# Optimization experiments

Measured on AMD Instinct MI355X. Metric: run time of the kernel, lower is better.

The kernel has to match this reference:

```python
import jax, jax.numpy as jnp
import numpy as np

DIM = 512
HEADS = 8
DK = DIM // HEADS
MAX_LEN = 22118
EPS = 1e-5


def _layernorm(h, g, b):
    m = jnp.mean(h, axis=-1, keepdims=True)
    v = jnp.mean((h - m) ** 2, axis=-1, keepdims=True)
    return (h - m) / jnp.sqrt(v + EPS) * g + b


def setup_inputs() -> dict:
    key = jax.random.key(0)
    ks = jax.random.split(key, 16)
    B, S = 4, 2048
    xavier = lambda k, shp: jax.random.normal(k, shp, jnp.float32) * np.sqrt(2.0 / (shp[0] + shp[1]))
    return {
        "x": jax.random.normal(ks[0], (B, S, DIM), jnp.float32),
        "vis_data": jax.random.normal(ks[1], (B, S, DIM), jnp.float32),
        "coord1": jax.random.randint(ks[2], (B, S), 0, MAX_LEN, jnp.int32),
        "coord2": jax.random.randint(ks[3], (B, S), 0, MAX_LEN, jnp.int32),
        "emb1": jax.random.normal(ks[4], (MAX_LEN, DIM // 2), jnp.float32) * 0.02,
        "emb2": jax.random.normal(ks[5], (MAX_LEN, DIM // 2), jnp.float32) * 0.02,
        "wq": xavier(ks[6], (DIM, DIM)), "bq": jnp.zeros((DIM,), jnp.float32),
        "wk": xavier(ks[7], (DIM, DIM)), "bk": jnp.zeros((DIM,), jnp.float32),
        "wv": xavier(ks[8], (DIM, DIM)), "bv": jnp.zeros((DIM,), jnp.float32),
        "w1": xavier(ks[9], (DIM, DIM)), "b1": jnp.zeros((DIM,), jnp.float32),
        "g1": jnp.ones((DIM,), jnp.float32), "beta1": jnp.zeros((DIM,), jnp.float32),
        "w2": xavier(ks[10], (DIM, DIM)), "b2": jnp.zeros((DIM,), jnp.float32),
        "g2": jnp.ones((DIM,), jnp.float32), "beta2": jnp.zeros((DIM,), jnp.float32),
    }


def reference(x, vis_data, coord1, coord2, emb1, emb2, wq, bq, wk, bk, wv, bv,
              w1, b1, g1, beta1, w2, b2, g2, beta2):
    B, S, _ = x.shape
    # learned positional encoding: concat of two coordinate embeddings
    pos = jnp.concatenate([emb1[coord1], emb2[coord2]], axis=-1)  # [B,S,DIM]
    xp = x + pos
    # Q/K from vis_data, V from position-encoded x
    q = (vis_data @ wq + bq).reshape(B, S, HEADS, DK)
    k = (vis_data @ wk + bk).reshape(B, S, HEADS, DK)
    v = (xp @ wv + bv).reshape(B, S, HEADS, DK)
    scores = jnp.einsum("bqhd,bkhd->bhqk", q, k) / np.sqrt(DK).astype(np.float32)
    attn = jax.nn.softmax(scores, axis=-1)  # dropout is identity in eval
    out = jnp.einsum("bhqk,bkhd->bqhd", attn, v).reshape(B, S, DIM)
    # post-attention MLP stack (self.layer)
    h = jax.nn.leaky_relu(out @ w1 + b1, negative_slope=0.2)
    h = _layernorm(h, g1, beta1)
    h = jax.nn.leaky_relu(h @ w2 + b2, negative_slope=0.2)
    h = _layernorm(h, g2, beta2)
    return h
```

## Files before the change

kernel.cpp:

```cpp
#include <hip/hip_runtime.h>

#define DIM 512
#define SEQ 2048
#define MROWS 8192

typedef short short8 __attribute__((ext_vector_type(8)));
typedef float floatx4 __attribute__((ext_vector_type(4)));

__device__ __forceinline__ ushort f2bf(float f) {
  union { float f; unsigned u; } v; v.f = f;
  unsigned r = v.u + 0x7fff + ((v.u >> 16) & 1);
  return (ushort)(r >> 16);
}
__device__ __forceinline__ float bf2f(ushort u) {
  union { unsigned u; float f; } v; v.u = ((unsigned)u) << 16;
  return v.f;
}

__global__ __launch_bounds__(256) void prep_kernel(
    const float* __restrict__ x, const float* __restrict__ vis,
    const int* __restrict__ c1, const int* __restrict__ c2,
    const float* __restrict__ e1, const float* __restrict__ e2,
    ushort* __restrict__ xp_bf, ushort* __restrict__ vis_bf) {
  int gid = blockIdx.x * 256 + threadIdx.x;
  int row = gid >> 7;
  int col = (gid & 127) * 4;
  float4 vv = *(const float4*)(vis + (size_t)row * 512 + col);
  ushort4 vb; vb.x = f2bf(vv.x); vb.y = f2bf(vv.y); vb.z = f2bf(vv.z); vb.w = f2bf(vv.w);
  *(ushort4*)(vis_bf + (size_t)row * 512 + col) = vb;
  float4 p;
  if (col < 256) p = *(const float4*)(e1 + (size_t)c1[row] * 256 + col);
  else           p = *(const float4*)(e2 + (size_t)c2[row] * 256 + col - 256);
  float4 xv = *(const float4*)(x + (size_t)row * 512 + col);
  ushort4 xb; xb.x = f2bf(xv.x + p.x); xb.y = f2bf(xv.y + p.y);
  xb.z = f2bf(xv.z + p.z); xb.w = f2bf(xv.w + p.w);
  *(ushort4*)(xp_bf + (size_t)row * 512 + col) = xb;
}

__global__ __launch_bounds__(256) void wtrans_kernel(
    const float* __restrict__ wq, const float* __restrict__ wk,
    const float* __restrict__ wv, const float* __restrict__ w1,
    const float* __restrict__ w2,
    ushort* __restrict__ wt_qkv, ushort* __restrict__ wt1,
    ushort* __restrict__ wt2) {
  __shared__ float Ls[64 * 65];
  int mid = blockIdx.x >> 6;
  int tile = blockIdx.x & 63;
  int k0 = (tile >> 3) * 64, n0 = (tile & 7) * 64;
  const float* W = mid == 0 ? wq : mid == 1 ? wk : mid == 2 ? wv : mid == 3 ? w1 : w2;
  ushort* outp = mid < 3 ? (wt_qkv + (size_t)mid * 512 * 512) : (mid == 3 ? wt1 : wt2);
  float scale = (mid == 0) ? 0.125f : 1.0f;
  int r = threadIdx.x >> 4, c4 = (threadIdx.x & 15) * 4;
#pragma unroll
  for (int i = 0; i < 4; i++) {
    int row = i * 16 + r;
    float4 wv4 = *(const float4*)(W + (size_t)(k0 + row) * 512 + n0 + c4);
    Ls[row * 65 + c4 + 0] = wv4.x * scale;
    Ls[row * 65 + c4 + 1] = wv4.y * scale;
    Ls[row * 65 + c4 + 2] = wv4.z * scale;
    Ls[row * 65 + c4 + 3] = wv4.w * scale;
  }
  __syncthreads();
  int n = threadIdx.x >> 2, kc = (threadIdx.x & 3) * 16;
  ushort pk[16];
#pragma unroll
  for (int i = 0; i < 16; i++) pk[i] = f2bf(Ls[(kc + i) * 65 + n]);
  ushort* op = outp + (size_t)(n0 + n) * 512 + k0 + kc;
  *(uint4*)op = *(uint4*)pk;
  *(uint4*)(op + 8) = *(uint4*)(pk + 8);
}

template <bool LEAKY>
__global__ __launch_bounds__(256, 3) void gemm_mfma(
    const ushort* __restrict__ A01, const ushort* __restrict__ A2,
    const ushort* __restrict__ Wt,
    const float* __restrict__ bias0, const float* __restrict__ bias1,
    const float* __restrict__ bias2,
    ushort* __restrict__ out0, ushort* __restrict__ out1,
    ushort* __restrict__ out2, float s0scale) {
  __shared__ __align__(16) ushort As[128 * 64];
  __shared__ __align__(16) ushort Bs[128 * 64];
  int t = threadIdx.x;
  int seg = blockIdx.x >> 2;
  int nloc0 = (blockIdx.x & 3) * 128;
  int n0w = blockIdx.x * 128;
  int m0 = blockIdx.y * 128;
  const ushort* A = (seg < 2) ? A01 : A2;
  const float* bias = seg == 0 ? bias0 : seg == 1 ? bias1 : bias2;
  ushort* out = seg == 0 ? out0 : seg == 1 ? out1 : out2;
  float bscale = seg == 0 ? s0scale : 1.0f;

  int w = t >> 6, lane = t & 63;
  int wm = (w & 1) * 64, wn = (w >> 1) * 64;
  int quad = lane >> 4, lcol = lane & 15;
  int srow = t >> 3, sch = t & 7;

  floatx4 acc[4][4] = {};

  for (int k0 = 0; k0 < 512; k0 += 64) {
    __syncthreads();
#pragma unroll
    for (int i = 0; i < 4; i++) {
      int row = i * 32 + srow;
      int pofs = row * 64 + (sch ^ (row & 7)) * 8;
      *(uint4*)(&As[pofs]) =
          *(const uint4*)(A + (size_t)(m0 + row) * 512 + k0 + sch * 8);
      *(uint4*)(&Bs[pofs]) =
          *(const uint4*)(Wt + (size_t)(n0w + row) * 512 + k0 + sch * 8);
    }
    __syncthreads();
#pragma unroll
    for (int kc = 0; kc < 2; kc++) {
      int pch = ((kc * 4 + quad) ^ (lcol & 7)) * 8;
      short8 af[4], bfr[4];
#pragma unroll
      for (int i = 0; i < 4; i++) {
        af[i]  = *(const short8*)(&As[(wm + i * 16 + lcol) * 64 + pch]);
        bfr[i] = *(const short8*)(&Bs[(wn + i * 16 + lcol) * 64 + pch]);
      }
#pragma unroll
      for (int mt = 0; mt < 4; mt++)
#pragma unroll
        for (int nt = 0; nt < 4; nt++)
          acc[mt][nt] = __builtin_amdgcn_mfma_f32_16x16x32_bf16(
              af[mt], bfr[nt], acc[mt][nt], 0, 0, 0);
    }
  }

  __syncthreads();
  float* Ls = ((w & 2) ? (float*)Bs : (float*)As) + (w & 1) * 1104;
  int rr = lane >> 2, cc = (lane & 3) * 16;
#pragma unroll
  for (int mt = 0; mt < 4; mt++) {
#pragma unroll
    for (int nt = 0; nt < 4; nt++) {
      float bv = bias[nloc0 + wn + nt * 16 + lcol] * bscale;
#pragma unroll
      for (int r = 0; r < 4; r++) {
        float vv = acc[mt][nt][r] + bv;
        if (LEAKY) vv = vv >= 0.f ? vv : 0.2f * vv;
        Ls[(quad * 4 + r) * 68 + nt * 16 + lcol] = vv;
      }
    }
    asm volatile("s_waitcnt lgkmcnt(0)" ::: "memory");
    ushort pk[16];
#pragma unroll
    for (int i = 0; i < 16; i += 4) {
      float4 fv = *(const float4*)(&Ls[rr * 68 + cc + i]);
      pk[i] = f2bf(fv.x); pk[i + 1] = f2bf(fv.y);
      pk[i + 2] = f2bf(fv.z); pk[i + 3] = f2bf(fv.w);
    }
    ushort* op = out + (size_t)(m0 + wm + mt * 16 + rr) * 512 + nloc0 + wn + cc;
    *(uint4*)op = *(uint4*)pk;
    *(uint4*)(op + 8) = *(uint4*)(pk + 8);
    asm volatile("s_waitcnt lgkmcnt(0)" ::: "memory");
  }
}

__global__ __launch_bounds__(256, 4) void attn_mfma_kernel(
    const ushort* __restrict__ q, const ushort* __restrict__ k,
    const ushort* __restrict__ v, ushort* __restrict__ out) {
  __shared__ __align__(16) ushort Ks[128 * 64];
  __shared__ __align__(16) ushort Vt[64 * 128];
  __shared__ __align__(16) ushort Ps[4 * 16 * 64];
  int t = threadIdx.x;
  int blk = blockIdx.x;
  int qt = blk & 31, h = (blk >> 5) & 7, b = blk >> 8;
  int wave = t >> 6, lane = t & 63, quad = lane >> 4, lcol = lane & 15;
  int q0 = qt * 64 + wave * 16;
  const size_t base = (size_t)b * SEQ * 512 + h * 64;

  short8 qf[2];
#pragma unroll
  for (int kc = 0; kc < 2; kc++)
    qf[kc] = *(const short8*)(q + base + (size_t)(q0 + lcol) * 512 + kc * 32 + quad * 8);

  floatx4 O[4] = {};
  float lsum[4] = {0.f, 0.f, 0.f, 0.f};

  ushort* Pw = Ps + wave * (16 * 64);
  int krow = t >> 1, khalf = t & 1;
  int pl = t & 63, dg = t >> 6;

  for (int kt = 0; kt < SEQ; kt += 128) {
    __syncthreads();
#pragma unroll
    for (int j = 0; j < 4; j++) {
      int ch = khalf * 4 + j;
      *(uint4*)(&Ks[krow * 64 + (ch ^ (krow & 7)) * 8]) =
          *(const uint4*)(k + base + (size_t)(kt + krow) * 512 + ch * 8);
    }
    {
      uint4 va[2], vb[2];
      const ushort* vr0 = v + base + (size_t)(kt + 2 * pl) * 512 + dg * 16;
      const ushort* vr1 = vr0 + 512;
      va[0] = *(const uint4*)(vr0); va[1] = *(const uint4*)(vr0 + 8);
      vb[0] = *(const uint4*)(vr1); vb[1] = *(const uint4*)(vr1 + 8);
      const ushort* a0 = (const ushort*)va;
      const ushort* a1 = (const ushort*)vb;
#pragma unroll
      for (int i = 0; i < 16; i++) {
        int dim = dg * 16 + i;
        unsigned pack = (unsigned)a0[i] | ((unsigned)a1[i] << 16);
        int pch = (pl >> 2) ^ (dim & 7);
        *(unsigned*)(&Vt[dim * 128 + pch * 8 + (pl & 3) * 2]) = pack;
      }
    }
    __syncthreads();

    floatx4 S[8] = {};
#pragma unroll
    for (int kc = 0; kc < 2; kc++) {
      int pch = ((kc * 4 + quad) ^ (lcol & 7)) * 8;
#pragma unroll
      for (int jt = 0; jt < 8; jt++) {
        short8 kf = *(const short8*)(&Ks[(jt * 16 + lcol) * 64 + pch]);
        S[jt] = __builtin_amdgcn_mfma_f32_16x16x32_bf16(qf[kc], kf, S[jt], 0, 0, 0);
      }
    }

#pragma unroll
    for (int half = 0; half < 2; half++) {
#pragma unroll
      for (int jt4 = 0; jt4 < 4; jt4++) {
        int jt = half * 4 + jt4;
#pragma unroll
        for (int r = 0; r < 4; r++) {
          float p = __expf(S[jt][r]);
          lsum[r] += p;
          int prow = quad * 4 + r;
          int pcol = jt4 * 16 + lcol;
          int pch = (pcol >> 3) ^ (prow & 7);
          Pw[prow * 64 + pch * 8 + (pcol & 7)] =
              (ushort)(__float_as_uint(p) >> 16);
        }
      }
      asm volatile("s_waitcnt lgkmcnt(0)" ::: "memory");
#pragma unroll
      for (int kc = 0; kc < 2; kc++) {
        short8 pf = *(const short8*)(
            &Pw[lcol * 64 + ((kc * 4 + quad) ^ (lcol & 7)) * 8]);
#pragma unroll
        for (int nt = 0; nt < 4; nt++) {
          int dim = nt * 16 + lcol;
          int ch = half * 8 + kc * 4 + quad;
          short8 vf = *(const short8*)(&Vt[dim * 128 + (ch ^ (lcol & 7)) * 8]);
          O[nt] = __builtin_amdgcn_mfma_f32_16x16x32_bf16(pf, vf, O[nt], 0, 0, 0);
        }
      }
    }
  }

#pragma unroll
  for (int r = 0; r < 4; r++) {
#pragma unroll
    for (int m = 1; m <= 8; m <<= 1) lsum[r] += __shfl_xor(lsum[r], m, 64);
    lsum[r] = 1.f / lsum[r];
  }
#pragma unroll
  for (int nt = 0; nt < 4; nt++)
#pragma unroll
    for (int r = 0; r < 4; r++)
      out[base + (size_t)(q0 + quad * 4 + r) * 512 + nt * 16 + lcol] =
          f2bf(O[nt][r] * lsum[r]);
}

template <bool OUTF32>
__global__ __launch_bounds__(256) void ln_kernel(
    const ushort* __restrict__ h, const float* __restrict__ g,
    const float* __restrict__ beta, void* __restrict__ outv) {
  int wave = threadIdx.x >> 6, lane = threadIdx.x & 63;
  int row = blockIdx.x * 4 + wave;
  uint4 raw = *(const uint4*)(h + (size_t)row * 512 + lane * 8);
  const ushort* hu = (const ushort*)&raw;
  float vals[8];
#pragma unroll
  for (int i = 0; i < 8; i++) vals[i] = bf2f(hu[i]);
  float sum = 0.f;
#pragma unroll
  for (int i = 0; i < 8; i++) sum += vals[i];
#pragma unroll
  for (int off = 32; off >= 1; off >>= 1) sum += __shfl_xor(sum, off, 64);
  float mean = sum * (1.f / 512.f);
  float vs = 0.f;
#pragma unroll
  for (int i = 0; i < 8; i++) { float d = vals[i] - mean; vs += d * d; }
#pragma unroll
  for (int off = 32; off >= 1; off >>= 1) vs += __shfl_xor(vs, off, 64);
  float rstd = rsqrtf(vs * (1.f / 512.f) + 1e-5f);
  float4 gv0 = *(const float4*)(g + lane * 8);
  float4 gv1 = *(const float4*)(g + lane * 8 + 4);
  float4 bv0 = *(const float4*)(beta + lane * 8);
  float4 bv1 = *(const float4*)(beta + lane * 8 + 4);
  float gr[8] = {gv0.x, gv0.y, gv0.z, gv0.w, gv1.x, gv1.y, gv1.z, gv1.w};
  float br[8] = {bv0.x, bv0.y, bv0.z, bv0.w, bv1.x, bv1.y, bv1.z, bv1.w};
  float res[8];
#pragma unroll
  for (int i = 0; i < 8; i++) res[i] = (vals[i] - mean) * rstd * gr[i] + br[i];
  if (OUTF32) {
    float* op = (float*)outv + (size_t)row * 512 + lane * 8;
    float4 o0, o1;
    o0.x = res[0]; o0.y = res[1]; o0.z = res[2]; o0.w = res[3];
    o1.x = res[4]; o1.y = res[5]; o1.z = res[6]; o1.w = res[7];
    *(float4*)op = o0; *(float4*)(op + 4) = o1;
  } else {
    ushort* op = (ushort*)outv + (size_t)row * 512 + lane * 8;
    ushort4 o0, o1;
    o0.x = f2bf(res[0]); o0.y = f2bf(res[1]); o0.z = f2bf(res[2]); o0.w = f2bf(res[3]);
    o1.x = f2bf(res[4]); o1.y = f2bf(res[5]); o1.z = f2bf(res[6]); o1.w = f2bf(res[7]);
    *(ushort4*)op = o0; *(ushort4*)(op + 4) = o1;
  }
}

extern "C" void kernel_launch(void* const* d_in, const int* in_sizes, int n_in,
                              void* d_out, int out_size, void* d_ws,
                              size_t ws_size, hipStream_t stream) {
  (void)in_sizes; (void)n_in; (void)out_size; (void)ws_size;
  const float* x     = (const float*)d_in[0];
  const float* vis   = (const float*)d_in[1];
  const int*   c1    = (const int*)d_in[2];
  const int*   c2    = (const int*)d_in[3];
  const float* e1    = (const float*)d_in[4];
  const float* e2    = (const float*)d_in[5];
  const float* wq    = (const float*)d_in[6];
  const float* bq    = (const float*)d_in[7];
  const float* wk    = (const float*)d_in[8];
  const float* bk    = (const float*)d_in[9];
  const float* wv    = (const float*)d_in[10];
  const float* bv    = (const float*)d_in[11];
  const float* w1    = (const float*)d_in[12];
  const float* b1    = (const float*)d_in[13];
  const float* g1    = (const float*)d_in[14];
  const float* beta1 = (const float*)d_in[15];
  const float* w2    = (const float*)d_in[16];
  const float* b2    = (const float*)d_in[17];
  const float* g2    = (const float*)d_in[18];
  const float* beta2 = (const float*)d_in[19];
  float* out = (float*)d_out;
  ushort* ws = (ushort*)d_ws;

  const size_t BUF = (size_t)MROWS * 512;
  ushort* xp_bf  = ws;
  ushort* vis_bf = ws + BUF;
  ushort* q_bf   = ws + 2 * BUF;
  ushort* k_bf   = ws + 3 * BUF;
  ushort* v_bf   = ws + 4 * BUF;
  ushort* wt_qkv = ws + 5 * BUF;
  ushort* wt1    = wt_qkv + 1536 * 512;
  ushort* wt2    = wt1 + 512 * 512;
  ushort* attn_bf = vis_bf;
  ushort* h1_bf   = xp_bf;
  ushort* ln1_bf  = q_bf;
  ushort* h2_bf   = k_bf;

  prep_kernel<<<4096, 256, 0, stream>>>(x, vis, c1, c2, e1, e2, xp_bf, vis_bf);
  wtrans_kernel<<<320, 256, 0, stream>>>(wq, wk, wv, w1, w2, wt_qkv, wt1, wt2);
  gemm_mfma<false><<<dim3(12, 64), 256, 0, stream>>>(
      vis_bf, xp_bf, wt_qkv, bq, bk, bv, q_bf, k_bf, v_bf, 0.125f);
  attn_mfma_kernel<<<1024, 256, 0, stream>>>(q_bf, k_bf, v_bf, attn_bf);
  gemm_mfma<true><<<dim3(4, 64), 256, 0, stream>>>(
      attn_bf, attn_bf, wt1, b1, b1, b1, h1_bf, h1_bf, h1_bf, 1.0f);
  ln_kernel<false><<<2048, 256, 0, stream>>>(h1_bf, g1, beta1, ln1_bf);
  gemm_mfma<true><<<dim3(4, 64), 256, 0, stream>>>(
      ln1_bf, ln1_bf, wt2, b2, b2, b2, h2_bf, h2_bf, h2_bf, 1.0f);
  ln_kernel<true><<<2048, 256, 0, stream>>>(h2_bf, g2, beta2, out);
}
```

Measured before the change: 308.1 us.

## Merge prep kernels, split-K MLP GEMMs with fused LN, widen attention query tile

New measurement: 290.1 us. -5.8%, faster.

```diff
diff --git a/kernel.cpp b/kernel.cpp
--- a/kernel.cpp
+++ b/kernel.cpp
@@ -17,60 +17,60 @@
   return v.f;
 }
 
-__global__ __launch_bounds__(256) void prep_kernel(
+__global__ __launch_bounds__(256) void prep_wtrans_kernel(
     const float* __restrict__ x, const float* __restrict__ vis,
     const int* __restrict__ c1, const int* __restrict__ c2,
     const float* __restrict__ e1, const float* __restrict__ e2,
-    ushort* __restrict__ xp_bf, ushort* __restrict__ vis_bf) {
-  int gid = blockIdx.x * 256 + threadIdx.x;
-  int row = gid >> 7;
-  int col = (gid & 127) * 4;
-  float4 vv = *(const float4*)(vis + (size_t)row * 512 + col);
-  ushort4 vb; vb.x = f2bf(vv.x); vb.y = f2bf(vv.y); vb.z = f2bf(vv.z); vb.w = f2bf(vv.w);
-  *(ushort4*)(vis_bf + (size_t)row * 512 + col) = vb;
-  float4 p;
-  if (col < 256) p = *(const float4*)(e1 + (size_t)c1[row] * 256 + col);
-  else           p = *(const float4*)(e2 + (size_t)c2[row] * 256 + col - 256);
-  float4 xv = *(const float4*)(x + (size_t)row * 512 + col);
-  ushort4 xb; xb.x = f2bf(xv.x + p.x); xb.y = f2bf(xv.y + p.y);
-  xb.z = f2bf(xv.z + p.z); xb.w = f2bf(xv.w + p.w);
-  *(ushort4*)(xp_bf + (size_t)row * 512 + col) = xb;
-}
-
-__global__ __launch_bounds__(256) void wtrans_kernel(
     const float* __restrict__ wq, const float* __restrict__ wk,
     const float* __restrict__ wv, const float* __restrict__ w1,
     const float* __restrict__ w2,
+    ushort* __restrict__ xp_bf, ushort* __restrict__ vis_bf,
     ushort* __restrict__ wt_qkv, ushort* __restrict__ wt1,
     ushort* __restrict__ wt2) {
   __shared__ float Ls[64 * 65];
-  int mid = blockIdx.x >> 6;
-  int tile = blockIdx.x & 63;
-  int k0 = (tile >> 3) * 64, n0 = (tile & 7) * 64;
-  const float* W = mid == 0 ? wq : mid == 1 ? wk : mid == 2 ? wv : mid == 3 ? w1 : w2;
-  ushort* outp = mid < 3 ? (wt_qkv + (size_t)mid * 512 * 512) : (mid == 3 ? wt1 : wt2);
-  float scale = (mid == 0) ? 0.125f : 1.0f;
-  int r = threadIdx.x >> 4, c4 = (threadIdx.x & 15) * 4;
-#pragma unroll
-  for (int i = 0; i < 4; i++) {
-    int row = i * 16 + r;
-    float4 wv4 = *(const float4*)(W + (size_t)(k0 + row) * 512 + n0 + c4);
-    Ls[row * 65 + c4 + 0] = wv4.x * scale;
-    Ls[row * 65 + c4 + 1] = wv4.y * scale;
-    Ls[row * 65 + c4 + 2] = wv4.z * scale;
-    Ls[row * 65 + c4 + 3] = wv4.w * scale;
-  }
-  __syncthreads();
-  int n = threadIdx.x >> 2, kc = (threadIdx.x & 3) * 16;
-  ushort pk[16];
-#pragma unroll
-  for (int i = 0; i < 16; i++) pk[i] = f2bf(Ls[(kc + i) * 65 + n]);
-  ushort* op = outp + (size_t)(n0 + n) * 512 + k0 + kc;
-  *(uint4*)op = *(uint4*)pk;
-  *(uint4*)(op + 8) = *(uint4*)(pk + 8);
-}
-
-template <bool LEAKY>
+  if (blockIdx.x < 4096) {
+    int gid = blockIdx.x * 256 + threadIdx.x;
+    int row = gid >> 7;
+    int col = (gid & 127) * 4;
+    float4 vv = *(const float4*)(vis + (size_t)row * 512 + col);
+    ushort4 vb; vb.x = f2bf(vv.x); vb.y = f2bf(vv.y); vb.z = f2bf(vv.z); vb.w = f2bf(vv.w);
+    *(ushort4*)(vis_bf + (size_t)row * 512 + col) = vb;
+    float4 p;
+    if (col < 256) p = *(const float4*)(e1 + (size_t)c1[row] * 256 + col);
+    else           p = *(const float4*)(e2 + (size_t)c2[row] * 256 + col - 256);
+    float4 xv = *(const float4*)(x + (size_t)row * 512 + col);
+    ushort4 xb; xb.x = f2bf(xv.x + p.x); xb.y = f2bf(xv.y + p.y);
+    xb.z = f2bf(xv.z + p.z); xb.w = f2bf(xv.w + p.w);
+    *(ushort4*)(xp_bf + (size_t)row * 512 + col) = xb;
+  } else {
+    int bid = blockIdx.x - 4096;
+    int mid = bid >> 6;
+    int tile = bid & 63;
+    int k0 = (tile >> 3) * 64, n0 = (tile & 7) * 64;
+    const float* W = mid == 0 ? wq : mid == 1 ? wk : mid == 2 ? wv : mid == 3 ? w1 : w2;
+    ushort* outp = mid < 3 ? (wt_qkv + (size_t)mid * 512 * 512) : (mid == 3 ? wt1 : wt2);
+    float scale = (mid == 0) ? 0.125f : 1.0f;
+    int r = threadIdx.x >> 4, c4 = (threadIdx.x & 15) * 4;
+#pragma unroll
+    for (int i = 0; i < 4; i++) {
+      int row = i * 16 + r;
+      float4 wv4 = *(const float4*)(W + (size_t)(k0 + row) * 512 + n0 + c4);
+      Ls[row * 65 + c4 + 0] = wv4.x * scale;
+      Ls[row * 65 + c4 + 1] = wv4.y * scale;
+      Ls[row * 65 + c4 + 2] = wv4.z * scale;
+      Ls[row * 65 + c4 + 3] = wv4.w * scale;
+    }
+    __syncthreads();
+    int n = threadIdx.x >> 2, kc = (threadIdx.x & 3) * 16;
+    ushort pk[16];
+#pragma unroll
+    for (int i = 0; i < 16; i++) pk[i] = f2bf(Ls[(kc + i) * 65 + n]);
+    ushort* op = outp + (size_t)(n0 + n) * 512 + k0 + kc;
+    *(uint4*)op = *(uint4*)pk;
+    *(uint4*)(op + 8) = *(uint4*)(pk + 8);
+  }
+}
+
 __global__ __launch_bounds__(256, 3) void gemm_mfma(
     const ushort* __restrict__ A01, const ushort* __restrict__ A2,
     const ushort* __restrict__ Wt,
@@ -136,11 +136,8 @@
     for (int nt = 0; nt < 4; nt++) {
       float bv = bias[nloc0 + wn + nt * 16 + lcol] * bscale;
 #pragma unroll
-      for (int r = 0; r < 4; r++) {
-        float vv = acc[mt][nt][r] + bv;
-        if (LEAKY) vv = vv >= 0.f ? vv : 0.2f * vv;
-        Ls[(quad * 4 + r) * 68 + nt * 16 + lcol] = vv;
-      }
+      for (int r = 0; r < 4; r++)
+        Ls[(quad * 4 + r) * 68 + nt * 16 + lcol] = acc[mt][nt][r] + bv;
     }
     asm volatile("s_waitcnt lgkmcnt(0)" ::: "memory");
     ushort pk[16];
@@ -157,28 +154,97 @@
   }
 }
 
-__global__ __launch_bounds__(256, 4) void attn_mfma_kernel(
+__global__ __launch_bounds__(256, 3) void gemm_splitk(
+    const ushort* __restrict__ A, const ushort* __restrict__ Wt,
+    float* __restrict__ P0, float* __restrict__ P1) {
+  __shared__ __align__(16) ushort As[128 * 64];
+  __shared__ __align__(16) ushort Bs[128 * 64];
+  int t = threadIdx.x;
+  int nt0 = (blockIdx.x & 3) * 128;
+  int khalf = blockIdx.x >> 2;
+  int m0 = blockIdx.y * 128;
+  float* Pout = khalf ? P1 : P0;
+  int w = t >> 6, lane = t & 63;
+  int wm = (w & 1) * 64, wn = (w >> 1) * 64;
+  int quad = lane >> 4, lcol = lane & 15;
+  int srow = t >> 3, sch = t & 7;
+  floatx4 acc[4][4] = {};
+  int kbase = khalf * 256;
+
+  for (int k0 = kbase; k0 < kbase + 256; k0 += 64) {
+    __syncthreads();
+#pragma unroll
+    for (int i = 0; i < 4; i++) {
+      int row = i * 32 + srow;
+      int pofs = row * 64 + (sch ^ (row & 7)) * 8;
+      *(uint4*)(&As[pofs]) =
+          *(const uint4*)(A + (size_t)(m0 + row) * 512 + k0 + sch * 8);
+      *(uint4*)(&Bs[pofs]) =
+          *(const uint4*)(Wt + (size_t)(nt0 + row) * 512 + k0 + sch * 8);
+    }
+    __syncthreads();
+#pragma unroll
+    for (int kc = 0; kc < 2; kc++) {
+      int pch = ((kc * 4 + quad) ^ (lcol & 7)) * 8;
+      short8 af[4], bfr[4];
+#pragma unroll
+      for (int i = 0; i < 4; i++) {
+        af[i]  = *(const short8*)(&As[(wm + i * 16 + lcol) * 64 + pch]);
+        bfr[i] = *(const short8*)(&Bs[(wn + i * 16 + lcol) * 64 + pch]);
+      }
+#pragma unroll
+      for (int mt = 0; mt < 4; mt++)
+#pragma unroll
+        for (int nt = 0; nt < 4; nt++)
+          acc[mt][nt] = __builtin_amdgcn_mfma_f32_16x16x32_bf16(
+              af[mt], bfr[nt], acc[mt][nt], 0, 0, 0);
+    }
+  }
+
+  __syncthreads();
+  float* Ls = ((w & 2) ? (float*)Bs : (float*)As) + (w & 1) * 1104;
+  int rr = lane >> 2, cc = (lane & 3) * 16;
+#pragma unroll
+  for (int mt = 0; mt < 4; mt++) {
+#pragma unroll
+    for (int nt = 0; nt < 4; nt++)
+#pragma unroll
+      for (int r = 0; r < 4; r++)
+        Ls[(quad * 4 + r) * 68 + nt * 16 + lcol] = acc[mt][nt][r];
+    asm volatile("s_waitcnt lgkmcnt(0)" ::: "memory");
+    float* op = Pout + (size_t)(m0 + wm + mt * 16 + rr) * 512 + nt0 + wn + cc;
+#pragma unroll
+    for (int i = 0; i < 16; i += 4)
+      *(float4*)(op + i) = *(const float4*)(&Ls[rr * 68 + cc + i]);
+    asm volatile("s_waitcnt lgkmcnt(0)" ::: "memory");
+  }
+}
+
+__global__ __launch_bounds__(256, 2) void attn_mfma_kernel(
     const ushort* __restrict__ q, const ushort* __restrict__ k,
     const ushort* __restrict__ v, ushort* __restrict__ out) {
   __shared__ __align__(16) ushort Ks[128 * 64];
   __shared__ __align__(16) ushort Vt[64 * 128];
-  __shared__ __align__(16) ushort Ps[4 * 16 * 64];
+  __shared__ __align__(16) ushort Ps[4 * 32 * 64];
   int t = threadIdx.x;
   int blk = blockIdx.x;
-  int qt = blk & 31, h = (blk >> 5) & 7, b = blk >> 8;
+  int qt = blk & 15, h = (blk >> 4) & 7, b = blk >> 7;
   int wave = t >> 6, lane = t & 63, quad = lane >> 4, lcol = lane & 15;
-  int q0 = qt * 64 + wave * 16;
+  int q0 = qt * 128 + wave * 32;
   const size_t base = (size_t)b * SEQ * 512 + h * 64;
 
-  short8 qf[2];
-#pragma unroll
-  for (int kc = 0; kc < 2; kc++)
-    qf[kc] = *(const short8*)(q + base + (size_t)(q0 + lcol) * 512 + kc * 32 + quad * 8);
-
-  floatx4 O[4] = {};
-  float lsum[4] = {0.f, 0.f, 0.f, 0.f};
-
-  ushort* Pw = Ps + wave * (16 * 64);
+  short8 qf[2][2];
+#pragma unroll
+  for (int qm = 0; qm < 2; qm++)
+#pragma unroll
+    for (int kc = 0; kc < 2; kc++)
+      qf[qm][kc] = *(const short8*)(
+          q + base + (size_t)(q0 + qm * 16 + lcol) * 512 + kc * 32 + quad * 8);
+
+  floatx4 O[2][4] = {};
+  float lsum[2][4] = {};
+
+  ushort* Pw = Ps + wave * (32 * 64);
   int krow = t >> 1, khalf = t & 1;
   int pl = t & 63, dg = t >> 6;
 
@@ -208,74 +274,93 @@
     }
     __syncthreads();
 
-    floatx4 S[8] = {};
-#pragma unroll
-    for (int kc = 0; kc < 2; kc++) {
-      int pch = ((kc * 4 + quad) ^ (lcol & 7)) * 8;
-#pragma unroll
-      for (int jt = 0; jt < 8; jt++) {
-        short8 kf = *(const short8*)(&Ks[(jt * 16 + lcol) * 64 + pch]);
-        S[jt] = __builtin_amdgcn_mfma_f32_16x16x32_bf16(qf[kc], kf, S[jt], 0, 0, 0);
+#pragma unroll
+    for (int half = 0; half < 2; half++) {
+#pragma unroll
+      for (int qm = 0; qm < 2; qm++) {
+        floatx4 S[4] = {};
+#pragma unroll
+        for (int kc = 0; kc < 2; kc++) {
+          int pch = ((kc * 4 + quad) ^ (lcol & 7)) * 8;
+#pragma unroll
+          for (int jt4 = 0; jt4 < 4; jt4++) {
+            int jrow = (half * 4 + jt4) * 16 + lcol;
+            short8 kf = *(const short8*)(&Ks[jrow * 64 + pch]);
+            S[jt4] = __builtin_amdgcn_mfma_f32_16x16x32_bf16(
+                qf[qm][kc], kf, S[jt4], 0, 0, 0);
+          }
+        }
+#pragma unroll
+        for (int jt4 = 0; jt4 < 4; jt4++)
+#pragma unroll
+          for (int r = 0; r < 4; r++) {
+            float p = __expf(S[jt4][r]);
+            lsum[qm][r] += p;
+            int prow = qm * 16 + quad * 4 + r;
+            int pcol = jt4 * 16 + lcol;
+            int pch2 = (pcol >> 3) ^ (prow & 7);
+            Pw[prow * 64 + pch2 * 8 + (pcol & 7)] =
+                (ushort)(__float_as_uint(p) >> 16);
+          }
       }
-    }
-
-#pragma unroll
-    for (int half = 0; half < 2; half++) {
-#pragma unroll
-      for (int jt4 = 0; jt4 < 4; jt4++) {
-        int jt = half * 4 + jt4;
-#pragma unroll
-        for (int r = 0; r < 4; r++) {
-          float p = __expf(S[jt][r]);
-          lsum[r] += p;
-          int prow = quad * 4 + r;
-          int pcol = jt4 * 16 + lcol;
-          int pch = (pcol >> 3) ^ (prow & 7);
-          Pw[prow * 64 + pch * 8 + (pcol & 7)] =
-              (ushort)(__float_as_uint(p) >> 16);
+      asm volatile("s_waitcnt lgkmcnt(0)" ::: "memory");
+#pragma unroll
+      for (int qm = 0; qm < 2; qm++) {
+#pragma unroll
+        for (int kc = 0; kc < 2; kc++) {
+          short8 pf = *(const short8*)(
+              &Pw[(qm * 16 + lcol) * 64 + ((kc * 4 + quad) ^ (lcol & 7)) * 8]);
+#pragma unroll
+          for (int nt = 0; nt < 4; nt++) {
+            int dim = nt * 16 + lcol;
+            int ch = half * 8 + kc * 4 + quad;
+            short8 vf = *(const short8*)(&Vt[dim * 128 + (ch ^ (lcol & 7)) * 8]);
+            O[qm][nt] = __builtin_amdgcn_mfma_f32_16x16x32_bf16(
+                pf, vf, O[qm][nt], 0, 0, 0);
+          }
         }
       }
-      asm volatile("s_waitcnt lgkmcnt(0)" ::: "memory");
-#pragma unroll
-      for (int kc = 0; kc < 2; kc++) {
-        short8 pf = *(const short8*)(
-            &Pw[lcol * 64 + ((kc * 4 + quad) ^ (lcol & 7)) * 8]);
-#pragma unroll
-        for (int nt = 0; nt < 4; nt++) {
-          int dim = nt * 16 + lcol;
-          int ch = half * 8 + kc * 4 + quad;
-          short8 vf = *(const short8*)(&Vt[dim * 128 + (ch ^ (lcol & 7)) * 8]);
-          O[nt] = __builtin_amdgcn_mfma_f32_16x16x32_bf16(pf, vf, O[nt], 0, 0, 0);
-        }
-      }
-    }
-  }
-
-#pragma unroll
-  for (int r = 0; r < 4; r++) {
-#pragma unroll
-    for (int m = 1; m <= 8; m <<= 1) lsum[r] += __shfl_xor(lsum[r], m, 64);
-    lsum[r] = 1.f / lsum[r];
-  }
-#pragma unroll
-  for (int nt = 0; nt < 4; nt++)
-#pragma unroll
-    for (int r = 0; r < 4; r++)
-      out[base + (size_t)(q0 + quad * 4 + r) * 512 + nt * 16 + lcol] =
-          f2bf(O[nt][r] * lsum[r]);
+    }
+  }
+
+#pragma unroll
+  for (int qm = 0; qm < 2; qm++)
+#pragma unroll
+    for (int r = 0; r < 4; r++) {
+#pragma unroll
+      for (int m = 1; m <= 8; m <<= 1)
+        lsum[qm][r] += __shfl_xor(lsum[qm][r], m, 64);
+      lsum[qm][r] = 1.f / lsum[qm][r];
+    }
+#pragma unroll
+  for (int qm = 0; qm < 2; qm++)
+#pragma unroll
+    for (int nt = 0; nt < 4; nt++)
+#pragma unroll
+      for (int r = 0; r < 4; r++)
+        out[base + (size_t)(q0 + qm * 16 + quad * 4 + r) * 512 + nt * 16 + lcol] =
+            f2bf(O[qm][nt][r] * lsum[qm][r]);
 }
 
 template <bool OUTF32>
-__global__ __launch_bounds__(256) void ln_kernel(
-    const ushort* __restrict__ h, const float* __restrict__ g,
+__global__ __launch_bounds__(256) void ln_fuse(
+    const float* __restrict__ P0, const float* __restrict__ P1,
+    const float* __restrict__ bias, const float* __restrict__ g,
     const float* __restrict__ beta, void* __restrict__ outv) {
   int wave = threadIdx.x >> 6, lane = threadIdx.x & 63;
   int row = blockIdx.x * 4 + wave;
-  uint4 raw = *(const uint4*)(h + (size_t)row * 512 + lane * 8);
-  const ushort* hu = (const ushort*)&raw;
-  float vals[8];
-#pragma unroll
-  for (int i = 0; i < 8; i++) vals[i] = bf2f(hu[i]);
+  const float* p0 = P0 + (size_t)row * 512 + lane * 8;
+  const float* p1 = P1 + (size_t)row * 512 + lane * 8;
+  float4 a0 = *(const float4*)(p0), a1 = *(const float4*)(p0 + 4);
+  float4 b0 = *(const float4*)(p1), b1 = *(const float4*)(p1 + 4);
+  float4 c0 = *(const float4*)(bias + lane * 8);
+  float4 c1 = *(const float4*)(bias + lane * 8 + 4);
+  float vals[8] = {a0.x + b0.x + c0.x, a0.y + b0.y + c0.y,
+                   a0.z + b0.z + c0.z, a0.w + b0.w + c0.w,
+                   a1.x + b1.x + c1.x, a1.y + b1.y + c1.y,
+                   a1.z + b1.z + c1.z, a1.w + b1.w + c1.w};
+#pragma unroll
+  for (int i = 0; i < 8; i++) vals[i] = vals[i] >= 0.f ? vals[i] : 0.2f * vals[i];
   float sum = 0.f;
 #pragma unroll
   for (int i = 0; i < 8; i++) sum += vals[i];
@@ -345,23 +430,21 @@
   ushort* q_bf   = ws + 2 * BUF;
   ushort* k_bf   = ws + 3 * BUF;
   ushort* v_bf   = ws + 4 * BUF;
-  ushort* wt_qkv = ws + 5 * BUF;
+  float*  P0     = (float*)(ws + 2 * BUF);
+  float*  P1     = (float*)(ws + 4 * BUF);
+  ushort* wt_qkv = ws + 6 * BUF;
   ushort* wt1    = wt_qkv + 1536 * 512;
   ushort* wt2    = wt1 + 512 * 512;
   ushort* attn_bf = vis_bf;
-  ushort* h1_bf   = xp_bf;
-  ushort* ln1_bf  = q_bf;
-  ushort* h2_bf   = k_bf;
-
-  prep_kernel<<<4096, 256, 0, stream>>>(x, vis, c1, c2, e1, e2, xp_bf, vis_bf);
-  wtrans_kernel<<<320, 256, 0, stream>>>(wq, wk, wv, w1, w2, wt_qkv, wt1, wt2);
-  gemm_mfma<false><<<dim3(12, 64), 256, 0, stream>>>(
+  ushort* ln1_bf  = xp_bf;
+
+  prep_wtrans_kernel<<<4416, 256, 0, stream>>>(
+      x, vis, c1, c2, e1, e2, wq, wk, wv, w1, w2, xp_bf, vis_bf, wt_qkv, wt1, wt2);
+  gemm_mfma<<<dim3(12, 64), 256, 0, stream>>>(
       vis_bf, xp_bf, wt_qkv, bq, bk, bv, q_bf, k_bf, v_bf, 0.125f);
-  attn_mfma_kernel<<<1024, 256, 0, stream>>>(q_bf, k_bf, v_bf, attn_bf);
-  gemm_mfma<true><<<dim3(4, 64), 256, 0, stream>>>(
-      attn_bf, attn_bf, wt1, b1, b1, b1, h1_bf, h1_bf, h1_bf, 1.0f);
-  ln_kernel<false><<<2048, 256, 0, stream>>>(h1_bf, g1, beta1, ln1_bf);
-  gemm_mfma<true><<<dim3(4, 64), 256, 0, stream>>>(
-      ln1_bf, ln1_bf, wt2, b2, b2, b2, h2_bf, h2_bf, h2_bf, 1.0f);
-  ln_kernel<true><<<2048, 256, 0, stream>>>(h2_bf, g2, beta2, out);
-}
+  attn_mfma_kernel<<<512, 256, 0, stream>>>(q_bf, k_bf, v_bf, attn_bf);
+  gemm_splitk<<<dim3(8, 64), 256, 0, stream>>>(attn_bf, wt1, P0, P1);
+  ln_fuse<false><<<2048, 256, 0, stream>>>(P0, P1, b1, g1, beta1, ln1_bf);
+  gemm_splitk<<<dim3(8, 64), 256, 0, stream>>>(ln1_bf, wt2, P0, P1);
+  ln_fuse<true><<<2048, 256, 0, stream>>>(P0, P1, b2, g2, beta2, out);
+}
```
